# Kernel optimization log

Hardware: AMD Instinct MI355X
Metric: run time of the kernel (lower is better)

The kernel has to match this reference:

```python
import jax, jax.numpy as jnp
import numpy as np

B, D, H, DOUT, E, K = 8192, 1024, 4096, 1024, 8, 2


def setup_inputs() -> dict:
    key = jax.random.key(0)
    ks = jax.random.split(key, 7)
    s_d = 1.0 / np.sqrt(D)
    s_h = 1.0 / np.sqrt(H)
    return {
        "x": jax.random.normal(ks[0], (B, D), jnp.float32),
        "Wg": jax.random.uniform(ks[1], (D, E), jnp.float32, -s_d, s_d),
        "bg": jax.random.uniform(ks[2], (E,), jnp.float32, -s_d, s_d),
        "W1": jax.random.uniform(ks[3], (E, D, H), jnp.float32, -s_d, s_d),
        "b1": jax.random.uniform(ks[4], (E, H), jnp.float32, -s_d, s_d),
        "W2": jax.random.uniform(ks[5], (E, H, DOUT), jnp.float32, -s_h, s_h),
        "b2": jax.random.uniform(ks[6], (E, DOUT), jnp.float32, -s_h, s_h),
    }


def reference(x, Wg, bg, W1, b1, W2, b2):
    # gating
    gate_probs = jax.nn.softmax(x @ Wg + bg, axis=-1)          # [B, E]
    top_k_probs, top_k_idx = jax.lax.top_k(gate_probs, K)       # [B, K]
    top_k_probs = top_k_probs / jnp.sum(top_k_probs, axis=-1, keepdims=True)

    # dense all-expert compute (faithful to torch.stack over experts)
    h = jax.nn.gelu(jnp.einsum('bd,edh->beh', x, W1) + b1, approximate=False)  # [B, E, H]
    expert_outputs = jnp.einsum('beh,eho->beo', h, W2) + b2                    # [B, E, DOUT]

    # gather selected experts and combine
    sel = jnp.take_along_axis(expert_outputs, top_k_idx[:, :, None], axis=1)   # [B, K, DOUT]
    output = jnp.sum(sel * top_k_probs[:, :, None], axis=1)                    # [B, DOUT]

    # load-balancing aux loss (as written in the original)
    expert_usage = jnp.mean(gate_probs, axis=0)                # [E]
    uniform = jnp.full_like(expert_usage, 1.0 / E)
    aux_loss = jnp.sum(expert_usage * jnp.log(uniform) - jnp.log(expert_usage) * uniform)
    return output, aux_loss
```

## Files before the change

kernel.cpp:

```cpp
#include <hip/hip_runtime.h>
#include <hip/hip_bf16.h>
#include <hip/hip_fp16.h>

#define B_    8192
#define D_    1024
#define H_    4096
#define DOUT_ 1024
#define E_    8
#define MAXR  17408

typedef float    f32x4 __attribute__((ext_vector_type(4)));
typedef _Float16 f16x8 __attribute__((ext_vector_type(8)));
typedef unsigned short u16;
typedef u16      u16x8 __attribute__((ext_vector_type(8)));
typedef u16      u16x4 __attribute__((ext_vector_type(4)));
typedef unsigned int u32;

__device__ __forceinline__ u16 f2h_bits(float f) {
  _Float16 h = (_Float16)f;
  return __builtin_bit_cast(u16, h);
}

__device__ __forceinline__ float gelu_f(float v) {
  float z = 0.7978845608028654f * (v + 0.044715f * v * v * v);
  float ez = __expf(2.f * z);
  float th = 1.f - 2.f / (ez + 1.f);
  return 0.5f * v * (1.f + th);
}

#define OFF_TOPI 512
#define OFF_TOPW (OFF_TOPI + 65536)
#define OFF_ATOK (OFF_TOPW + 65536)
#define OFF_WSL  (OFF_ATOK + 69632)
#define OFF_XG   524288
#define OFF_W1T  (OFF_XG + 35651584)
#define OFF_W2T  OFF_XG
#define OFF_HB   (OFF_W1T + 67108864)

__global__ void k_zero_out(float* __restrict__ out) {
  size_t i = (size_t)(blockIdx.x * 256 + threadIdx.x) * 4;
  *(f32x4*)&out[i] = (f32x4){0.f, 0.f, 0.f, 0.f};
}

__global__ void k_init(int* __restrict__ atok, float* __restrict__ wslot,
                       int* __restrict__ meta) {
  int i = blockIdx.x * 256 + threadIdx.x;
  if (i < MAXR) { atok[i] = 0; wslot[i] = 0.f; }
  if (blockIdx.x == 0 && threadIdx.x < 64) meta[threadIdx.x] = 0;
}

__global__ __launch_bounds__(256) void k_gate(
    const float* __restrict__ x, const float* __restrict__ Wg,
    const float* __restrict__ bg, int* __restrict__ counts,
    float* __restrict__ usage, int* __restrict__ topi, float* __restrict__ topw) {
  __shared__ float su[E_];
  if (threadIdx.x < E_) su[threadIdx.x] = 0.f;
  __syncthreads();
  const int lane = threadIdx.x & 63;
  const int b = blockIdx.x * 4 + (threadIdx.x >> 6);
  float p[E_] = {0.f,0.f,0.f,0.f,0.f,0.f,0.f,0.f};
  #pragma unroll
  for (int j = 0; j < 4; ++j) {
    int d = j * 256 + lane * 4;
    float4 xv = *(const float4*)&x[(size_t)b * D_ + d];
    const float* wr = &Wg[(size_t)d * E_];
    #pragma unroll
    for (int c = 0; c < 4; ++c) {
      float xc = reinterpret_cast<const float*>(&xv)[c];
      #pragma unroll
      for (int e = 0; e < E_; ++e) p[e] += xc * wr[c * E_ + e];
    }
  }
  #pragma unroll
  for (int off = 32; off >= 1; off >>= 1)
    #pragma unroll
    for (int e = 0; e < E_; ++e) p[e] += __shfl_xor(p[e], off, 64);
  float mx = -1e30f;
  #pragma unroll
  for (int e = 0; e < E_; ++e) { p[e] += bg[e]; mx = fmaxf(mx, p[e]); }
  int i0 = 0; float l0 = p[0];
  #pragma unroll
  for (int e = 1; e < E_; ++e) if (p[e] > l0) { l0 = p[e]; i0 = e; }
  int i1 = -1; float l1 = -1e30f;
  #pragma unroll
  for (int e = 0; e < E_; ++e) if (e != i0 && p[e] > l1) { l1 = p[e]; i1 = e; }
  float s = 0.f;
  #pragma unroll
  for (int e = 0; e < E_; ++e) { p[e] = expf(p[e] - mx); s += p[e]; }
  float inv = 1.f / s;
  if (lane == 0) {
    float e0 = expf(l0 - mx), e1 = expf(l1 - mx);
    float wsum = e0 + e1;
    topi[b * 2] = i0; topi[b * 2 + 1] = i1;
    topw[b * 2] = e0 / wsum; topw[b * 2 + 1] = e1 / wsum;
    atomicAdd(&counts[i0], 1);
    atomicAdd(&counts[i1], 1);
    #pragma unroll
    for (int e = 0; e < E_; ++e) atomicAdd(&su[e], p[e] * inv);
  }
  __syncthreads();
  if (threadIdx.x < E_) atomicAdd(&usage[threadIdx.x], su[threadIdx.x]);
}

__global__ void k_scan_aux(const int* __restrict__ counts, int* __restrict__ offsets,
                           const float* __restrict__ usage, float* __restrict__ auxp) {
  if (threadIdx.x == 0) {
    int off = 0;
    for (int e = 0; e < E_; ++e) { offsets[e] = off; off += (counts[e] + 127) & ~127; }
    offsets[E_] = off;
    float aux = 0.f;
    const float lu = logf(1.0f / (float)E_);
    for (int e = 0; e < E_; ++e) {
      float u = usage[e] * (1.0f / (float)B_);
      aux += u * lu - logf(u) * (1.0f / (float)E_);
    }
    *auxp = aux;
  }
}

__global__ void k_scatter(const int* __restrict__ topi, const float* __restrict__ topw,
                          const int* __restrict__ offsets, int* __restrict__ cursors,
                          int* __restrict__ atok, float* __restrict__ wslot) {
  int b = blockIdx.x * 256 + threadIdx.x;
  if (b >= B_) return;
  #pragma unroll
  for (int k = 0; k < 2; ++k) {
    int e = topi[b * 2 + k];
    int pos = atomicAdd(&cursors[e], 1);
    int slot = offsets[e] + pos;
    atok[slot] = b;
    wslot[slot] = topw[b * 2 + k];
  }
}

__global__ __launch_bounds__(256) void k_gather(const float* __restrict__ x,
                                                const int* __restrict__ atok,
                                                u16* __restrict__ Xg) {
  int slot = blockIdx.x;
  int tok = atok[slot];
  int c = threadIdx.x * 4;
  float4 v = *(const float4*)&x[(size_t)tok * D_ + c];
  const float* vf = reinterpret_cast<const float*>(&v);
  u16x4 o;
  o.x = f2h_bits(vf[0]); o.y = f2h_bits(vf[1]);
  o.z = f2h_bits(vf[2]); o.w = f2h_bits(vf[3]);
  *(u16x4*)&Xg[(size_t)slot * D_ + c] = o;
}

__global__ __launch_bounds__(256) void k_cvt_t(const float* __restrict__ src,
                                               u16* __restrict__ dst, int K, int N) {
  const int e = blockIdx.z;
  const int kt = blockIdx.x * 64;
  const int nt = blockIdx.y * 64;
  __shared__ u16 t[64][68];
  const float* s = src + (size_t)e * K * N;
  u16* d = dst + (size_t)e * N * K;
  const int tr = threadIdx.x >> 4;
  const int tc = threadIdx.x & 15;
  #pragma unroll
  for (int i = 0; i < 4; ++i) {
    int k = tr + i * 16;
    float4 v = *(const float4*)&s[(size_t)(kt + k) * N + nt + tc * 4];
    t[k][tc*4+0] = f2h_bits(v.x); t[k][tc*4+1] = f2h_bits(v.y);
    t[k][tc*4+2] = f2h_bits(v.z); t[k][tc*4+3] = f2h_bits(v.w);
  }
  __syncthreads();
  #pragma unroll
  for (int i = 0; i < 4; ++i) {
    int n = tr + i * 16;
    u16x4 o;
    o.x = t[tc*4+0][n]; o.y = t[tc*4+1][n];
    o.z = t[tc*4+2][n]; o.w = t[tc*4+3][n];
    *(u16x4*)&d[(size_t)(nt + n) * K + kt + tc * 4] = o;
  }
}

#define GLDS(g, l) __builtin_amdgcn_global_load_lds( \
    (const u32 __attribute__((address_space(1)))*)(g), \
    (u32 __attribute__((address_space(3)))*)(l), 16, 0, 0)

#define STG(LDK, kk, Aoff, Boff) do { \
  const int r_ = lane >> 2; \
  const int sc_ = ((lane & 3) ^ ((r_ ^ (r_ >> 2)) & 3)) * 8; \
  _Pragma("unroll") \
  for (int c = 0; c < 2; ++c) { \
    int seg = wid * 2 + c; \
    GLDS(Ap + (size_t)(seg * 16 + r_) * (LDK) + (kk) + sc_, SM + (Aoff) + seg * 512); \
    GLDS(Bp + (size_t)(seg * 16 + r_) * (LDK) + (kk) + sc_, SM + (Boff) + seg * 512); \
  } } while (0)

#define CMP(Aoff, Boff) do { \
  const int r15_ = lane & 15; \
  const int co_ = (((lane >> 4) ^ ((r15_ ^ (r15_ >> 2)) & 3)) * 8); \
  f16x8 af[4], bf[4]; \
  _Pragma("unroll") \
  for (int m = 0; m < 4; ++m) \
    af[m] = *(const f16x8*)&SM[(Aoff) + (wr * 64 + m * 16 + r15_) * 32 + co_]; \
  _Pragma("unroll") \
  for (int n = 0; n < 4; ++n) \
    bf[n] = *(const f16x8*)&SM[(Boff) + (wc * 64 + n * 16 + r15_) * 32 + co_]; \
  _Pragma("unroll") \
  for (int m = 0; m < 4; ++m) \
    _Pragma("unroll") \
    for (int n = 0; n < 4; ++n) \
      acc[m][n] = __builtin_amdgcn_mfma_f32_16x16x32_f16(af[m], bf[n], acc[m][n], 0, 0, 0); \
  } while (0)

__global__ __launch_bounds__(256) void k_gemm1(
    const u16* __restrict__ Xg, const u16* __restrict__ W1t,
    const float* __restrict__ b1, const int* __restrict__ offsets,
    u16* __restrict__ Hb) {
  const int L = blockIdx.x;
  const int mtile = L >> 5;
  const int nt = L & 31;
  const int row0 = mtile * 128;
  if (row0 >= offsets[E_]) return;
  int e = 0;
  #pragma unroll
  for (int i = 1; i < E_; ++i) e = (row0 >= offsets[i]) ? i : e;
  const int n0 = nt * 128;
  const int tid = threadIdx.x, lane = tid & 63, wid = tid >> 6;
  const int wr = wid >> 1, wc = wid & 1;
  __shared__ __align__(16) u16 SM[16384];
  f32x4 acc[4][4] = {};
  const u16* Ap = Xg + (size_t)row0 * D_;
  const u16* Bp = W1t + (size_t)e * H_ * D_ + (size_t)n0 * D_;

  STG(D_, 0, 0, 4096);
  __syncthreads();
  for (int t = 0; t < 32; t += 2) {
    STG(D_, (t + 1) * 32, 8192, 12288);
    CMP(0, 4096);
    __syncthreads();
    if (t + 2 < 32) STG(D_, (t + 2) * 32, 0, 4096);
    CMP(8192, 12288);
    __syncthreads();
  }
  const int rhi = (lane >> 4) * 4, cix = lane & 15;
  float bv[4];
  #pragma unroll
  for (int n = 0; n < 4; ++n) bv[n] = b1[e * H_ + n0 + wc * 64 + n * 16 + cix];
  #pragma unroll
  for (int r = 0; r < 2; ++r) {
    if (wr == r) {
      #pragma unroll
      for (int m = 0; m < 4; ++m)
        #pragma unroll
        for (int n = 0; n < 4; ++n)
          #pragma unroll
          for (int j = 0; j < 4; ++j)
            SM[(m * 16 + rhi + j) * 136 + wc * 64 + n * 16 + cix] =
                f2h_bits(gelu_f(acc[m][n][j] + bv[n]));
    }
    __syncthreads();
    {
      const int rl = tid >> 2, co = (tid & 3) * 32;
      u16* dst = &Hb[(size_t)(row0 + r * 64 + rl) * H_ + n0 + co];
      const u16* srcp = &SM[rl * 136 + co];
      #pragma unroll
      for (int qq = 0; qq < 4; ++qq)
        *(u16x8*)(dst + qq * 8) = *(const u16x8*)(srcp + qq * 8);
    }
    __syncthreads();
  }
}

__global__ __launch_bounds__(256) void k_gemm2(
    const u16* __restrict__ Hb, const u16* __restrict__ W2t,
    const float* __restrict__ b2, const int* __restrict__ offsets,
    const int* __restrict__ atok, const float* __restrict__ wslot,
    float* __restrict__ out) {
  const int L = blockIdx.x;
  const int mtile = L >> 3;
  const int nt = L & 7;
  const int row0 = mtile * 128;
  if (row0 >= offsets[E_]) return;
  int e = 0;
  #pragma unroll
  for (int i = 1; i < E_; ++i) e = (row0 >= offsets[i]) ? i : e;
  const int n0 = nt * 128;
  const int tid = threadIdx.x, lane = tid & 63, wid = tid >> 6;
  const int wr = wid >> 1, wc = wid & 1;
  __shared__ __align__(16) u16 SM[16384];
  f32x4 acc[4][4] = {};
  const u16* Ap = Hb + (size_t)row0 * H_;
  const u16* Bp = W2t + (size_t)e * DOUT_ * H_ + (size_t)n0 * H_;

  STG(H_, 0, 0, 4096);
  __syncthreads();
  for (int t = 0; t < 128; t += 2) {
    STG(H_, (t + 1) * 32, 8192, 12288);
    CMP(0, 4096);
    __syncthreads();
    if (t + 2 < 128) STG(H_, (t + 2) * 32, 0, 4096);
    CMP(8192, 12288);
    __syncthreads();
  }
  const int rhi = (lane >> 4) * 4, cix = lane & 15;
  float bv[4];
  #pragma unroll
  for (int n = 0; n < 4; ++n) bv[n] = b2[e * DOUT_ + n0 + wc * 64 + n * 16 + cix];
  #pragma unroll
  for (int m = 0; m < 4; ++m) {
    #pragma unroll
    for (int j = 0; j < 4; ++j) {
      int slot = row0 + wr * 64 + m * 16 + rhi + j;
      float w = wslot[slot];
      if (w == 0.f) continue;
      int tok = atok[slot];
      float* orow = out + (size_t)tok * DOUT_ + n0;
      #pragma unroll
      for (int n = 0; n < 4; ++n) {
        int lc = wc * 64 + n * 16 + cix;
        atomicAdd(&orow[lc], w * (acc[m][n][j] + bv[n]));
      }
    }
  }
}

extern "C" void kernel_launch(void* const* d_in, const int* in_sizes, int n_in,
                              void* d_out, int out_size, void* d_ws, size_t ws_size,
                              hipStream_t stream) {
  const float* x  = (const float*)d_in[0];
  const float* Wg = (const float*)d_in[1];
  const float* bg = (const float*)d_in[2];
  const float* W1 = (const float*)d_in[3];
  const float* b1 = (const float*)d_in[4];
  const float* W2 = (const float*)d_in[5];
  const float* b2 = (const float*)d_in[6];
  float* out = (float*)d_out;

  char* ws = (char*)d_ws;
  int*   counts  = (int*)(ws + 0);
  int*   cursors = (int*)(ws + 32);
  int*   offsets = (int*)(ws + 64);
  float* usage   = (float*)(ws + 128);
  int*   topi    = (int*)(ws + OFF_TOPI);
  float* topw    = (float*)(ws + OFF_TOPW);
  int*   atok    = (int*)(ws + OFF_ATOK);
  float* wslot   = (float*)(ws + OFF_WSL);
  u16*   Xg      = (u16*)(ws + OFF_XG);
  u16*   W1t     = (u16*)(ws + OFF_W1T);
  u16*   W2t     = (u16*)(ws + OFF_W2T);
  u16*   Hb      = (u16*)(ws + OFF_HB);

  k_zero_out<<<B_ * DOUT_ / 1024, 256, 0, stream>>>(out);
  k_init<<<(MAXR + 255) / 256, 256, 0, stream>>>(atok, wslot, (int*)ws);
  k_gate<<<B_ / 4, 256, 0, stream>>>(x, Wg, bg, counts, usage, topi, topw);
  k_scan_aux<<<1, 64, 0, stream>>>(counts, offsets, usage, out + (size_t)B_ * DOUT_);
  k_scatter<<<B_ / 256, 256, 0, stream>>>(topi, topw, offsets, cursors, atok, wslot);
  k_gather<<<MAXR, 256, 0, stream>>>(x, atok, Xg);
  k_cvt_t<<<dim3(D_ / 64, H_ / 64, E_), 256, 0, stream>>>(W1, W1t, D_, H_);
  k_gemm1<<<(MAXR / 128) * 32, 256, 0, stream>>>(Xg, W1t, b1, offsets, Hb);
  k_cvt_t<<<dim3(H_ / 64, DOUT_ / 64, E_), 256, 0, stream>>>(W2, W2t, H_, DOUT_);
  k_gemm2<<<(MAXR / 128) * 8, 256, 0, stream>>>(Hb, W2t, b2, offsets, atok, wslot, out);
}
```

Measured before the change: 926.6 us.

## Enlarge MoE GEMM tiles to 256x256 with tile map and split-K for GEMM2

Both expert GEMMs move from 128x128 tiles with 256 threads to 256x256 tiles with 512 threads (8 waves, each owning 128x64). A per-expert tile map built in the scan kernel replaces the fixed m-tile grid, and row clamping plus bounds checks handle partial tiles. GEMM2 also splits K into two halves across blockIdx.y, with bias added only by the first half, and both halves atomically accumulate into the output. The larger tiles raise operand reuse per LDS load and cut redundant global traffic. The cost is higher register and LDS use per block, which lowers occupancy, plus some wasted work on padded tile rows and doubled atomic traffic in GEMM2.

```diff
diff --git a/kernel.cpp b/kernel.cpp
--- a/kernel.cpp
+++ b/kernel.cpp
@@ -8,6 +8,7 @@
 #define DOUT_ 1024
 #define E_    8
 #define MAXR  17408
+#define NT256 72
 
 typedef float    f32x4 __attribute__((ext_vector_type(4)));
 typedef _Float16 f16x8 __attribute__((ext_vector_type(8)));
@@ -32,6 +33,7 @@
 #define OFF_TOPW (OFF_TOPI + 65536)
 #define OFF_ATOK (OFF_TOPW + 65536)
 #define OFF_WSL  (OFF_ATOK + 69632)
+#define OFF_TMAP 280064
 #define OFF_XG   524288
 #define OFF_W1T  (OFF_XG + 35651584)
 #define OFF_W2T  OFF_XG
@@ -103,11 +105,19 @@
 }
 
 __global__ void k_scan_aux(const int* __restrict__ counts, int* __restrict__ offsets,
-                           const float* __restrict__ usage, float* __restrict__ auxp) {
+                           const float* __restrict__ usage, float* __restrict__ auxp,
+                           int* __restrict__ tmap) {
   if (threadIdx.x == 0) {
     int off = 0;
     for (int e = 0; e < E_; ++e) { offsets[e] = off; off += (counts[e] + 127) & ~127; }
     offsets[E_] = off;
+    int nT = 0;
+    for (int e = 0; e < E_; ++e) {
+      int roff = offsets[e], pn = offsets[e + 1] - roff;
+      for (int r0 = 0; r0 < pn; r0 += 256)
+        tmap[nT++] = (e << 20) | (roff + r0);
+    }
+    for (int t = nT; t < NT256; ++t) tmap[t] = -1;
     float aux = 0.f;
     const float lu = logf(1.0f / (float)E_);
     for (int e = 0; e < E_; ++e) {
@@ -185,55 +195,55 @@
   _Pragma("unroll") \
   for (int c = 0; c < 2; ++c) { \
     int seg = wid * 2 + c; \
-    GLDS(Ap + (size_t)(seg * 16 + r_) * (LDK) + (kk) + sc_, SM + (Aoff) + seg * 512); \
+    int rowA = seg * 16 + r_; if (rowA > Alim) rowA = Alim; \
+    GLDS(Ap + (size_t)rowA * (LDK) + (kk) + sc_, SM + (Aoff) + seg * 512); \
     GLDS(Bp + (size_t)(seg * 16 + r_) * (LDK) + (kk) + sc_, SM + (Boff) + seg * 512); \
   } } while (0)
 
 #define CMP(Aoff, Boff) do { \
   const int r15_ = lane & 15; \
   const int co_ = (((lane >> 4) ^ ((r15_ ^ (r15_ >> 2)) & 3)) * 8); \
-  f16x8 af[4], bf[4]; \
+  f16x8 af[8], bf[4]; \
   _Pragma("unroll") \
-  for (int m = 0; m < 4; ++m) \
-    af[m] = *(const f16x8*)&SM[(Aoff) + (wr * 64 + m * 16 + r15_) * 32 + co_]; \
+  for (int m = 0; m < 8; ++m) \
+    af[m] = *(const f16x8*)&SM[(Aoff) + (wr * 128 + m * 16 + r15_) * 32 + co_]; \
   _Pragma("unroll") \
   for (int n = 0; n < 4; ++n) \
     bf[n] = *(const f16x8*)&SM[(Boff) + (wc * 64 + n * 16 + r15_) * 32 + co_]; \
   _Pragma("unroll") \
-  for (int m = 0; m < 4; ++m) \
+  for (int m = 0; m < 8; ++m) \
     _Pragma("unroll") \
     for (int n = 0; n < 4; ++n) \
       acc[m][n] = __builtin_amdgcn_mfma_f32_16x16x32_f16(af[m], bf[n], acc[m][n], 0, 0, 0); \
   } while (0)
 
-__global__ __launch_bounds__(256) void k_gemm1(
+__global__ __launch_bounds__(512, 2) void k_gemm1(
     const u16* __restrict__ Xg, const u16* __restrict__ W1t,
     const float* __restrict__ b1, const int* __restrict__ offsets,
-    u16* __restrict__ Hb) {
-  const int L = blockIdx.x;
-  const int mtile = L >> 5;
-  const int nt = L & 31;
-  const int row0 = mtile * 128;
-  if (row0 >= offsets[E_]) return;
-  int e = 0;
-  #pragma unroll
-  for (int i = 1; i < E_; ++i) e = (row0 >= offsets[i]) ? i : e;
-  const int n0 = nt * 128;
+    const int* __restrict__ tmap, u16* __restrict__ Hb) {
+  const int packed = tmap[blockIdx.x >> 4];
+  if (packed < 0) return;
+  const int e = packed >> 20;
+  const int row0g = packed & 0xFFFFF;
+  const int rend = offsets[e + 1];
+  const int nt = blockIdx.x & 15;
+  const int n0 = nt * 256;
   const int tid = threadIdx.x, lane = tid & 63, wid = tid >> 6;
-  const int wr = wid >> 1, wc = wid & 1;
-  __shared__ __align__(16) u16 SM[16384];
-  f32x4 acc[4][4] = {};
-  const u16* Ap = Xg + (size_t)row0 * D_;
+  const int wr = wid >> 2, wc = wid & 3;
+  const int Alim = (MAXR - 1) - row0g;
+  __shared__ __align__(16) u16 SM[32768];
+  f32x4 acc[8][4] = {};
+  const u16* Ap = Xg + (size_t)row0g * D_;
   const u16* Bp = W1t + (size_t)e * H_ * D_ + (size_t)n0 * D_;
 
-  STG(D_, 0, 0, 4096);
+  STG(D_, 0, 0, 8192);
   __syncthreads();
   for (int t = 0; t < 32; t += 2) {
-    STG(D_, (t + 1) * 32, 8192, 12288);
-    CMP(0, 4096);
-    __syncthreads();
-    if (t + 2 < 32) STG(D_, (t + 2) * 32, 0, 4096);
-    CMP(8192, 12288);
+    STG(D_, (t + 1) * 32, 16384, 24576);
+    CMP(0, 8192);
+    __syncthreads();
+    if (t + 2 < 32) STG(D_, (t + 2) * 32, 0, 8192);
+    CMP(16384, 24576);
     __syncthreads();
   }
   const int rhi = (lane >> 4) * 4, cix = lane & 15;
@@ -241,70 +251,76 @@
   #pragma unroll
   for (int n = 0; n < 4; ++n) bv[n] = b1[e * H_ + n0 + wc * 64 + n * 16 + cix];
   #pragma unroll
-  for (int r = 0; r < 2; ++r) {
-    if (wr == r) {
+  for (int rr = 0; rr < 4; ++rr) {
+    if (wr == (rr >> 1)) {
+      const int mb = (rr & 1) * 4;
       #pragma unroll
       for (int m = 0; m < 4; ++m)
         #pragma unroll
         for (int n = 0; n < 4; ++n)
           #pragma unroll
           for (int j = 0; j < 4; ++j)
-            SM[(m * 16 + rhi + j) * 136 + wc * 64 + n * 16 + cix] =
-                f2h_bits(gelu_f(acc[m][n][j] + bv[n]));
+            SM[(m * 16 + rhi + j) * 264 + wc * 64 + n * 16 + cix] =
+                f2h_bits(gelu_f(acc[mb + m][n][j] + bv[n]));
     }
     __syncthreads();
     {
-      const int rl = tid >> 2, co = (tid & 3) * 32;
-      u16* dst = &Hb[(size_t)(row0 + r * 64 + rl) * H_ + n0 + co];
-      const u16* srcp = &SM[rl * 136 + co];
-      #pragma unroll
-      for (int qq = 0; qq < 4; ++qq)
-        *(u16x8*)(dst + qq * 8) = *(const u16x8*)(srcp + qq * 8);
-    }
-    __syncthreads();
-  }
-}
-
-__global__ __launch_bounds__(256) void k_gemm2(
+      const int rl = tid >> 3, co = (tid & 7) * 32;
+      const int gr = row0g + rr * 64 + rl;
+      if (gr < rend) {
+        u16* dst = &Hb[(size_t)gr * H_ + n0 + co];
+        const u16* sp = &SM[rl * 264 + co];
+        #pragma unroll
+        for (int qq = 0; qq < 4; ++qq)
+          *(u16x8*)(dst + qq * 8) = *(const u16x8*)(sp + qq * 8);
+      }
+    }
+    __syncthreads();
+  }
+}
+
+__global__ __launch_bounds__(512, 2) void k_gemm2(
     const u16* __restrict__ Hb, const u16* __restrict__ W2t,
     const float* __restrict__ b2, const int* __restrict__ offsets,
-    const int* __restrict__ atok, const float* __restrict__ wslot,
-    float* __restrict__ out) {
-  const int L = blockIdx.x;
-  const int mtile = L >> 3;
-  const int nt = L & 7;
-  const int row0 = mtile * 128;
-  if (row0 >= offsets[E_]) return;
-  int e = 0;
-  #pragma unroll
-  for (int i = 1; i < E_; ++i) e = (row0 >= offsets[i]) ? i : e;
-  const int n0 = nt * 128;
+    const int* __restrict__ tmap, const int* __restrict__ atok,
+    const float* __restrict__ wslot, float* __restrict__ out) {
+  const int packed = tmap[blockIdx.x >> 2];
+  if (packed < 0) return;
+  const int e = packed >> 20;
+  const int row0g = packed & 0xFFFFF;
+  const int rend = offsets[e + 1];
+  const int nt = blockIdx.x & 3;
+  const int n0 = nt * 256;
+  const int kbase = blockIdx.y * 2048;
   const int tid = threadIdx.x, lane = tid & 63, wid = tid >> 6;
-  const int wr = wid >> 1, wc = wid & 1;
-  __shared__ __align__(16) u16 SM[16384];
-  f32x4 acc[4][4] = {};
-  const u16* Ap = Hb + (size_t)row0 * H_;
-  const u16* Bp = W2t + (size_t)e * DOUT_ * H_ + (size_t)n0 * H_;
-
-  STG(H_, 0, 0, 4096);
-  __syncthreads();
-  for (int t = 0; t < 128; t += 2) {
-    STG(H_, (t + 1) * 32, 8192, 12288);
-    CMP(0, 4096);
-    __syncthreads();
-    if (t + 2 < 128) STG(H_, (t + 2) * 32, 0, 4096);
-    CMP(8192, 12288);
+  const int wr = wid >> 2, wc = wid & 3;
+  const int Alim = (MAXR - 1) - row0g;
+  __shared__ __align__(16) u16 SM[32768];
+  f32x4 acc[8][4] = {};
+  const u16* Ap = Hb + (size_t)row0g * H_ + kbase;
+  const u16* Bp = W2t + (size_t)e * DOUT_ * H_ + (size_t)n0 * H_ + kbase;
+
+  STG(H_, 0, 0, 8192);
+  __syncthreads();
+  for (int t = 0; t < 64; t += 2) {
+    STG(H_, (t + 1) * 32, 16384, 24576);
+    CMP(0, 8192);
+    __syncthreads();
+    if (t + 2 < 64) STG(H_, (t + 2) * 32, 0, 8192);
+    CMP(16384, 24576);
     __syncthreads();
   }
   const int rhi = (lane >> 4) * 4, cix = lane & 15;
+  const int first = (kbase == 0);
   float bv[4];
   #pragma unroll
   for (int n = 0; n < 4; ++n) bv[n] = b2[e * DOUT_ + n0 + wc * 64 + n * 16 + cix];
   #pragma unroll
-  for (int m = 0; m < 4; ++m) {
+  for (int m = 0; m < 8; ++m) {
     #pragma unroll
     for (int j = 0; j < 4; ++j) {
-      int slot = row0 + wr * 64 + m * 16 + rhi + j;
+      int slot = row0g + wr * 128 + m * 16 + rhi + j;
+      if (slot >= rend) continue;
       float w = wslot[slot];
       if (w == 0.f) continue;
       int tok = atok[slot];
@@ -312,7 +328,8 @@
       #pragma unroll
       for (int n = 0; n < 4; ++n) {
         int lc = wc * 64 + n * 16 + cix;
-        atomicAdd(&orow[lc], w * (acc[m][n][j] + bv[n]));
+        float v = first ? w * (acc[m][n][j] + bv[n]) : w * acc[m][n][j];
+        atomicAdd(&orow[lc], v);
       }
     }
   }
@@ -339,6 +356,7 @@
   float* topw    = (float*)(ws + OFF_TOPW);
   int*   atok    = (int*)(ws + OFF_ATOK);
   float* wslot   = (float*)(ws + OFF_WSL);
+  int*   tmap    = (int*)(ws + OFF_TMAP);
   u16*   Xg      = (u16*)(ws + OFF_XG);
   u16*   W1t     = (u16*)(ws + OFF_W1T);
   u16*   W2t     = (u16*)(ws + OFF_W2T);
@@ -347,11 +365,11 @@
   k_zero_out<<<B_ * DOUT_ / 1024, 256, 0, stream>>>(out);
   k_init<<<(MAXR + 255) / 256, 256, 0, stream>>>(atok, wslot, (int*)ws);
   k_gate<<<B_ / 4, 256, 0, stream>>>(x, Wg, bg, counts, usage, topi, topw);
-  k_scan_aux<<<1, 64, 0, stream>>>(counts, offsets, usage, out + (size_t)B_ * DOUT_);
+  k_scan_aux<<<1, 64, 0, stream>>>(counts, offsets, usage, out + (size_t)B_ * DOUT_, tmap);
   k_scatter<<<B_ / 256, 256, 0, stream>>>(topi, topw, offsets, cursors, atok, wslot);
   k_gather<<<MAXR, 256, 0, stream>>>(x, atok, Xg);
   k_cvt_t<<<dim3(D_ / 64, H_ / 64, E_), 256, 0, stream>>>(W1, W1t, D_, H_);
-  k_gemm1<<<(MAXR / 128) * 32, 256, 0, stream>>>(Xg, W1t, b1, offsets, Hb);
+  k_gemm1<<<NT256 * 16, 512, 0, stream>>>(Xg, W1t, b1, offsets, tmap, Hb);
   k_cvt_t<<<dim3(H_ / 64, DOUT_ / 64, E_), 256, 0, stream>>>(W2, W2t, H_, DOUT_);
-  k_gemm2<<<(MAXR / 128) * 8, 256, 0, stream>>>(Hb, W2t, b2, offsets, atok, wslot, out);
-}
+  k_gemm2<<<dim3(NT256 * 4, 2), 512, 0, stream>>>(Hb, W2t, b2, offsets, tmap, atok, wslot, out);
+}
```

After: 963.0 us. 3.9% more time.

## Use single-buffered BK=64 tiles with 8-way XOR swizzle in grouped GEMMs

Applied to the files above, without the earlier changes.

The K tile doubles from 32 to 64 per stage, and the double-buffered prefetch pipeline is replaced by a single buffer of the same LDS size: load, sync, compute, sync. The LDS swizzle becomes an 8-chunk XOR on the row index to match the 64-wide rows. This halves the number of barriers per K step and issues larger loads. In exchange, global loads no longer overlap MFMA compute within a block, so latency hiding now depends on other resident blocks.

```diff
diff --git a/kernel.cpp b/kernel.cpp
--- a/kernel.cpp
+++ b/kernel.cpp
@@ -180,31 +180,37 @@
     (u32 __attribute__((address_space(3)))*)(l), 16, 0, 0)
 
 #define STG(LDK, kk, Aoff, Boff) do { \
-  const int r_ = lane >> 2; \
-  const int sc_ = ((lane & 3) ^ ((r_ ^ (r_ >> 2)) & 3)) * 8; \
+  const int rl_ = lane >> 3; \
+  const int sc_ = ((lane & 7) ^ rl_) * 8; \
   _Pragma("unroll") \
-  for (int c = 0; c < 2; ++c) { \
-    int seg = wid * 2 + c; \
-    GLDS(Ap + (size_t)(seg * 16 + r_) * (LDK) + (kk) + sc_, SM + (Aoff) + seg * 512); \
-    GLDS(Bp + (size_t)(seg * 16 + r_) * (LDK) + (kk) + sc_, SM + (Boff) + seg * 512); \
+  for (int i = 0; i < 4; ++i) { \
+    int seg = wid * 4 + i; \
+    GLDS(Ap + (size_t)(seg * 8 + rl_) * (LDK) + (kk) + sc_, SM + (Aoff) + seg * 512); \
+    GLDS(Bp + (size_t)(seg * 8 + rl_) * (LDK) + (kk) + sc_, SM + (Boff) + seg * 512); \
   } } while (0)
 
 #define CMP(Aoff, Boff) do { \
   const int r15_ = lane & 15; \
-  const int co_ = (((lane >> 4) ^ ((r15_ ^ (r15_ >> 2)) & 3)) * 8); \
-  f16x8 af[4], bf[4]; \
+  const int hi_ = lane >> 4; \
   _Pragma("unroll") \
-  for (int m = 0; m < 4; ++m) \
-    af[m] = *(const f16x8*)&SM[(Aoff) + (wr * 64 + m * 16 + r15_) * 32 + co_]; \
-  _Pragma("unroll") \
-  for (int n = 0; n < 4; ++n) \
-    bf[n] = *(const f16x8*)&SM[(Boff) + (wc * 64 + n * 16 + r15_) * 32 + co_]; \
-  _Pragma("unroll") \
-  for (int m = 0; m < 4; ++m) \
+  for (int ks = 0; ks < 2; ++ks) { \
+    f16x8 af[4], bf[4]; \
     _Pragma("unroll") \
-    for (int n = 0; n < 4; ++n) \
-      acc[m][n] = __builtin_amdgcn_mfma_f32_16x16x32_f16(af[m], bf[n], acc[m][n], 0, 0, 0); \
-  } while (0)
+    for (int m = 0; m < 4; ++m) { \
+      int row = wr * 64 + m * 16 + r15_; \
+      af[m] = *(const f16x8*)&SM[(Aoff) + row * 64 + (((ks * 4 + hi_) ^ (row & 7)) * 8)]; \
+    } \
+    _Pragma("unroll") \
+    for (int n = 0; n < 4; ++n) { \
+      int row = wc * 64 + n * 16 + r15_; \
+      bf[n] = *(const f16x8*)&SM[(Boff) + row * 64 + (((ks * 4 + hi_) ^ (row & 7)) * 8)]; \
+    } \
+    _Pragma("unroll") \
+    for (int m = 0; m < 4; ++m) \
+      _Pragma("unroll") \
+      for (int n = 0; n < 4; ++n) \
+        acc[m][n] = __builtin_amdgcn_mfma_f32_16x16x32_f16(af[m], bf[n], acc[m][n], 0, 0, 0); \
+  } } while (0)
 
 __global__ __launch_bounds__(256) void k_gemm1(
     const u16* __restrict__ Xg, const u16* __restrict__ W1t,
@@ -226,14 +232,10 @@
   const u16* Ap = Xg + (size_t)row0 * D_;
   const u16* Bp = W1t + (size_t)e * H_ * D_ + (size_t)n0 * D_;
 
-  STG(D_, 0, 0, 4096);
-  __syncthreads();
-  for (int t = 0; t < 32; t += 2) {
-    STG(D_, (t + 1) * 32, 8192, 12288);
-    CMP(0, 4096);
-    __syncthreads();
-    if (t + 2 < 32) STG(D_, (t + 2) * 32, 0, 4096);
-    CMP(8192, 12288);
+  for (int t = 0; t < 16; ++t) {
+    STG(D_, t * 64, 0, 8192);
+    __syncthreads();
+    CMP(0, 8192);
     __syncthreads();
   }
   const int rhi = (lane >> 4) * 4, cix = lane & 15;
@@ -286,14 +288,10 @@
   const u16* Ap = Hb + (size_t)row0 * H_;
   const u16* Bp = W2t + (size_t)e * DOUT_ * H_ + (size_t)n0 * H_;
 
-  STG(H_, 0, 0, 4096);
-  __syncthreads();
-  for (int t = 0; t < 128; t += 2) {
-    STG(H_, (t + 1) * 32, 8192, 12288);
-    CMP(0, 4096);
-    __syncthreads();
-    if (t + 2 < 128) STG(H_, (t + 2) * 32, 0, 4096);
-    CMP(8192, 12288);
+  for (int t = 0; t < 64; ++t) {
+    STG(H_, t * 64, 0, 8192);
+    __syncthreads();
+    CMP(0, 8192);
     __syncthreads();
   }
   const int rhi = (lane >> 4) * 4, cix = lane & 15;
```

After: 982.7 us. 6.0% more time.

## Triple-buffer GEMM K-loop with vmcnt waits and split-K for second GEMM

Applied to the files above, without the earlier changes.

Both expert GEMMs move from a two-stage LDS double buffer with full __syncthreads to a three-stage ring buffer. Raw s_barrier plus explicit vmcnt waits let global-to-LDS loads run two tiles ahead of the MFMA work, and s_setprio raises priority around the MFMA block. The second GEMM is split along K into two halves on a second grid dimension, with only the first half adding the bias and both halves combining through atomics. This aims to hide memory latency and raise parallelism for the smaller GEMM, at the cost of more LDS per block (launch bounds ask for 3 blocks per CU) and twice as many atomic adds into the output.

```diff
diff --git a/kernel.cpp b/kernel.cpp
--- a/kernel.cpp
+++ b/kernel.cpp
@@ -179,34 +179,62 @@
     (const u32 __attribute__((address_space(1)))*)(g), \
     (u32 __attribute__((address_space(3)))*)(l), 16, 0, 0)
 
-#define STG(LDK, kk, Aoff, Boff) do { \
+#define VMWAIT(N) asm volatile("s_waitcnt vmcnt(" #N ")" ::: "memory")
+#define BARRIER() do { __builtin_amdgcn_s_barrier(); \
+                       asm volatile("" ::: "memory"); } while (0)
+
+#define NXT(x) ((x) == 16384 ? 0 : (x) + 8192)
+
+#define STG3(LDK, kt, sb) do { \
   const int r_ = lane >> 2; \
   const int sc_ = ((lane & 3) ^ ((r_ ^ (r_ >> 2)) & 3)) * 8; \
   _Pragma("unroll") \
-  for (int c = 0; c < 2; ++c) { \
-    int seg = wid * 2 + c; \
-    GLDS(Ap + (size_t)(seg * 16 + r_) * (LDK) + (kk) + sc_, SM + (Aoff) + seg * 512); \
-    GLDS(Bp + (size_t)(seg * 16 + r_) * (LDK) + (kk) + sc_, SM + (Boff) + seg * 512); \
+  for (int j = 0; j < 2; ++j) { \
+    int rw = j * 64 + wid * 16 + r_; \
+    GLDS(Ap + (size_t)rw * (LDK) + (kt) * 32 + sc_, SM + (sb) + j * 2048 + wid * 512); \
+    GLDS(Bp + (size_t)rw * (LDK) + (kt) * 32 + sc_, SM + (sb) + 4096 + j * 2048 + wid * 512); \
   } } while (0)
 
-#define CMP(Aoff, Boff) do { \
+#define RD_FR(rb_) do { \
   const int r15_ = lane & 15; \
   const int co_ = (((lane >> 4) ^ ((r15_ ^ (r15_ >> 2)) & 3)) * 8); \
-  f16x8 af[4], bf[4]; \
   _Pragma("unroll") \
-  for (int m = 0; m < 4; ++m) \
-    af[m] = *(const f16x8*)&SM[(Aoff) + (wr * 64 + m * 16 + r15_) * 32 + co_]; \
+  for (int mi = 0; mi < 4; ++mi) \
+    af[mi] = *(const f16x8*)&SM[(rb_) + (wr * 64 + mi * 16 + r15_) * 32 + co_]; \
   _Pragma("unroll") \
   for (int n = 0; n < 4; ++n) \
-    bf[n] = *(const f16x8*)&SM[(Boff) + (wc * 64 + n * 16 + r15_) * 32 + co_]; \
+    bf[n] = *(const f16x8*)&SM[(rb_) + 4096 + (wc * 64 + n * 16 + r15_) * 32 + co_]; \
+} while (0)
+
+#define MM16() do { \
+  __builtin_amdgcn_s_setprio(1); \
   _Pragma("unroll") \
-  for (int m = 0; m < 4; ++m) \
+  for (int mi = 0; mi < 4; ++mi) \
     _Pragma("unroll") \
     for (int n = 0; n < 4; ++n) \
-      acc[m][n] = __builtin_amdgcn_mfma_f32_16x16x32_f16(af[m], bf[n], acc[m][n], 0, 0, 0); \
-  } while (0)
-
-__global__ __launch_bounds__(256) void k_gemm1(
+      acc[mi][n] = __builtin_amdgcn_mfma_f32_16x16x32_f16(af[mi], bf[n], acc[mi][n], 0, 0, 0); \
+  __builtin_amdgcn_s_setprio(0); \
+} while (0)
+
+#define KLOOP(LDK, NT) do { \
+  int rb = 0, wb = 16384; \
+  STG3(LDK, 0, 0); \
+  STG3(LDK, 1, 8192); \
+  VMWAIT(4); \
+  BARRIER(); \
+  for (int t = 0; t < (NT); ++t) { \
+    RD_FR(rb); \
+    if (t + 2 < (NT)) STG3(LDK, t + 2, wb); \
+    BARRIER(); \
+    MM16(); \
+    if (t + 2 < (NT)) VMWAIT(4); \
+    else if (t + 1 < (NT)) VMWAIT(0); \
+    BARRIER(); \
+    rb = NXT(rb); wb = NXT(wb); \
+  } \
+} while (0)
+
+__global__ __launch_bounds__(256, 3) void k_gemm1(
     const u16* __restrict__ Xg, const u16* __restrict__ W1t,
     const float* __restrict__ b1, const int* __restrict__ offsets,
     u16* __restrict__ Hb) {
@@ -221,21 +249,14 @@
   const int n0 = nt * 128;
   const int tid = threadIdx.x, lane = tid & 63, wid = tid >> 6;
   const int wr = wid >> 1, wc = wid & 1;
-  __shared__ __align__(16) u16 SM[16384];
+  __shared__ __align__(16) u16 SM[24576];
   f32x4 acc[4][4] = {};
+  f16x8 af[4], bf[4];
   const u16* Ap = Xg + (size_t)row0 * D_;
   const u16* Bp = W1t + (size_t)e * H_ * D_ + (size_t)n0 * D_;
 
-  STG(D_, 0, 0, 4096);
-  __syncthreads();
-  for (int t = 0; t < 32; t += 2) {
-    STG(D_, (t + 1) * 32, 8192, 12288);
-    CMP(0, 4096);
-    __syncthreads();
-    if (t + 2 < 32) STG(D_, (t + 2) * 32, 0, 4096);
-    CMP(8192, 12288);
-    __syncthreads();
-  }
+  KLOOP(D_, 32);
+
   const int rhi = (lane >> 4) * 4, cix = lane & 15;
   float bv[4];
   #pragma unroll
@@ -265,7 +286,7 @@
   }
 }
 
-__global__ __launch_bounds__(256) void k_gemm2(
+__global__ __launch_bounds__(256, 3) void k_gemm2(
     const u16* __restrict__ Hb, const u16* __restrict__ W2t,
     const float* __restrict__ b2, const int* __restrict__ offsets,
     const int* __restrict__ atok, const float* __restrict__ wslot,
@@ -279,24 +300,19 @@
   #pragma unroll
   for (int i = 1; i < E_; ++i) e = (row0 >= offsets[i]) ? i : e;
   const int n0 = nt * 128;
+  const int kbase = blockIdx.y * 2048;
   const int tid = threadIdx.x, lane = tid & 63, wid = tid >> 6;
   const int wr = wid >> 1, wc = wid & 1;
-  __shared__ __align__(16) u16 SM[16384];
+  __shared__ __align__(16) u16 SM[24576];
   f32x4 acc[4][4] = {};
-  const u16* Ap = Hb + (size_t)row0 * H_;
-  const u16* Bp = W2t + (size_t)e * DOUT_ * H_ + (size_t)n0 * H_;
-
-  STG(H_, 0, 0, 4096);
-  __syncthreads();
-  for (int t = 0; t < 128; t += 2) {
-    STG(H_, (t + 1) * 32, 8192, 12288);
-    CMP(0, 4096);
-    __syncthreads();
-    if (t + 2 < 128) STG(H_, (t + 2) * 32, 0, 4096);
-    CMP(8192, 12288);
-    __syncthreads();
-  }
+  f16x8 af[4], bf[4];
+  const u16* Ap = Hb + (size_t)row0 * H_ + kbase;
+  const u16* Bp = W2t + (size_t)e * DOUT_ * H_ + (size_t)n0 * H_ + kbase;
+
+  KLOOP(H_, 64);
+
   const int rhi = (lane >> 4) * 4, cix = lane & 15;
+  const int first = (kbase == 0);
   float bv[4];
   #pragma unroll
   for (int n = 0; n < 4; ++n) bv[n] = b2[e * DOUT_ + n0 + wc * 64 + n * 16 + cix];
@@ -312,7 +328,8 @@
       #pragma unroll
       for (int n = 0; n < 4; ++n) {
         int lc = wc * 64 + n * 16 + cix;
-        atomicAdd(&orow[lc], w * (acc[m][n][j] + bv[n]));
+        float v = first ? w * (acc[m][n][j] + bv[n]) : w * acc[m][n][j];
+        atomicAdd(&orow[lc], v);
       }
     }
   }
@@ -353,5 +370,5 @@
   k_cvt_t<<<dim3(D_ / 64, H_ / 64, E_), 256, 0, stream>>>(W1, W1t, D_, H_);
   k_gemm1<<<(MAXR / 128) * 32, 256, 0, stream>>>(Xg, W1t, b1, offsets, Hb);
   k_cvt_t<<<dim3(H_ / 64, DOUT_ / 64, E_), 256, 0, stream>>>(W2, W2t, H_, DOUT_);
-  k_gemm2<<<(MAXR / 128) * 8, 256, 0, stream>>>(Hb, W2t, b2, offsets, atok, wslot, out);
-}
+  k_gemm2<<<dim3((MAXR / 128) * 8, 2), 256, 0, stream>>>(Hb, W2t, b2, offsets, atok, wslot, out);
+}
```

Result: faster. 836.0 us (-9.8%).
